# Performance work log

Hardware: AMD Instinct MI355X
Metric: run time of the kernel (lower is better)

## Reference

```python
import jax, jax.numpy as jnp
import numpy as np

B, S, D = 4, 4096, 1024

def setup_inputs() -> dict:
    key = jax.random.key(0)
    ks = jax.random.split(key, 7)
    scale = 1.0 / np.sqrt(D)
    X  = jax.random.normal(ks[0], (B, S, D), dtype=jnp.float32)
    Wq = jax.random.normal(ks[1], (D, D), dtype=jnp.float32) * scale
    bq = jnp.zeros((D,), dtype=jnp.float32)
    Wk = jax.random.normal(ks[2], (D, D), dtype=jnp.float32) * scale
    bk = jnp.zeros((D,), dtype=jnp.float32)
    Wv = jax.random.normal(ks[3], (D, D), dtype=jnp.float32) * scale
    bv = jnp.zeros((D,), dtype=jnp.float32)
    return {"X": X, "Wq": Wq, "bq": bq, "Wk": Wk, "bk": bk, "Wv": Wv, "bv": bv}

def reference(X, Wq, bq, Wk, bk, Wv, bv):
    # Linear projections (torch Linear: x @ W.T + b; here W stored as [D_in, D_out])
    Q = jnp.einsum('bsd,de->bse', X, Wq) + bq
    K = jnp.einsum('bsd,de->bse', X, Wk) + bk
    V = jnp.einsum('bsd,de->bse', X, Wv) + bv
    inv_sqrt_d = 1.0 / jnp.sqrt(jnp.float32(X.shape[-1]))
    scores = jnp.einsum('bqd,bkd->bqk', Q, K) * inv_sqrt_d  # [B,S,S]
    weights = jax.nn.sigmoid(scores)  # elementwise, no row normalization
    return jnp.einsum('bqk,bkd->bqd', weights, V)
```

## Files before the change

### kernel.cpp

```cpp
#include <hip/hip_runtime.h>
#include <hip/hip_bf16.h>

typedef __bf16 bf16_t;
typedef bf16_t bf16x8 __attribute__((ext_vector_type(8)));
typedef float f32x4 __attribute__((ext_vector_type(4)));

constexpr int D_DIM = 1024;
constexpr int S_DIM = 4096;
constexpr int B_DIM = 4;

__global__ void cast_f32_bf16(const float* __restrict__ in, bf16_t* __restrict__ out) {
  size_t i = ((size_t)blockIdx.x * blockDim.x + threadIdx.x) * 8;
  float4 a = *(const float4*)(in + i);
  float4 b = *(const float4*)(in + i + 4);
  bf16x8 o;
  o[0] = (bf16_t)a.x; o[1] = (bf16_t)a.y; o[2] = (bf16_t)a.z; o[3] = (bf16_t)a.w;
  o[4] = (bf16_t)b.x; o[5] = (bf16_t)b.y; o[6] = (bf16_t)b.z; o[7] = (bf16_t)b.w;
  *(bf16x8*)(out + i) = o;
}

__global__ void transpose_cast_1024(const float* __restrict__ in, bf16_t* __restrict__ out) {
  __shared__ float t[32][33];
  int x0 = blockIdx.x * 32, y0 = blockIdx.y * 32;
#pragma unroll
  for (int i = 0; i < 32; i += 8)
    t[threadIdx.y + i][threadIdx.x] =
        in[(size_t)(y0 + threadIdx.y + i) * D_DIM + (x0 + threadIdx.x)];
  __syncthreads();
#pragma unroll
  for (int i = 0; i < 32; i += 8)
    out[(size_t)(x0 + threadIdx.y + i) * D_DIM + (y0 + threadIdx.x)] =
        (bf16_t)t[threadIdx.x][threadIdx.y + i];
}

constexpr int BM2 = 256, BN2 = 256;

#define VMCNT8 asm volatile("s_waitcnt vmcnt(8)" ::: "memory")
#define VMCNT4 asm volatile("s_waitcnt vmcnt(4)" ::: "memory")
#define VMCNT0 asm volatile("s_waitcnt vmcnt(0)" ::: "memory")
#define LGKM8  asm volatile("s_waitcnt lgkmcnt(8)" ::: "memory")
#define LGKM0  asm volatile("s_waitcnt lgkmcnt(0)" ::: "memory")
#define SCHEDB __builtin_amdgcn_sched_barrier(0)
#define CFENCE asm volatile("" ::: "memory")
#define BAR __builtin_amdgcn_s_barrier()
#define PRIO1 __builtin_amdgcn_s_setprio(1)
#define PRIO0 __builtin_amdgcn_s_setprio(0)

__device__ __forceinline__ void stage_tile32(const bf16_t* __restrict__ g, int ld,
                                             bf16_t* lds, int tid) {
  const int w = tid >> 6, l = tid & 63;
  const int row = w * 16 + (l >> 2);
  const int chunk = (l & 3) * 8;
  const bf16_t* s0 = g + (size_t)row * ld + chunk;
  bf16_t* l0 = lds + w * 512;
  __builtin_amdgcn_global_load_lds((const __attribute__((address_space(1))) void*)s0,
                                   (__attribute__((address_space(3))) void*)l0, 16, 0, 0);
  __builtin_amdgcn_global_load_lds(
      (const __attribute__((address_space(1))) void*)(s0 + (size_t)128 * ld),
      (__attribute__((address_space(3))) void*)(l0 + 4096), 16, 0, 0);
}

template <int EPI, bool SWAP>
__global__ __launch_bounds__(512, 2) void gemm256k32(
    const bf16_t* __restrict__ A, const bf16_t* __restrict__ Bt,
    void* __restrict__ C0, void* __restrict__ C1, void* __restrict__ C2,
    const float* __restrict__ b0, const float* __restrict__ b1, const float* __restrict__ b2,
    int K, int lda, int ldb, int ldc, float scale,
    size_t sA, size_t sB, size_t sC) {
  __shared__ __align__(16) bf16_t smem[65536];

  const int tid = threadIdx.x;
  const int lane = tid & 63;
  const int w = tid >> 6;
  const int wr = (w >> 2) * 128;
  const int wc = (w & 3) * 64;
  const int fm = lane & 15;
  const int fko = (lane >> 4) * 8;

  const int nx = gridDim.x, ny = gridDim.y;
  const int nwg = nx * ny * gridDim.z;
  const int flat = blockIdx.x + nx * (blockIdx.y + ny * blockIdx.z);
  const int q = nwg >> 3;
  const int L = (flat & 7) * q + (flat >> 3);
  const int lx = L % nx;
  const int lt = L / nx;
  const int ly = lt % ny;
  const int lz = lt / ny;

  const int bx = SWAP ? ly : lx;
  const int by = SWAP ? lx : ly;

  const bf16_t* Ag = A + (size_t)lz * sA + (size_t)by * BM2 * lda;
  const bf16_t* Bg = Bt + (size_t)lz * sB + (size_t)bx * BN2 * ldb;

  f32x4 acc[8][4] = {};
  bf16x8 af[8], bfr[4];

  const int NT = K / 32;

  stage_tile32(Ag, lda, smem, tid);
  stage_tile32(Bg, ldb, smem + 8192, tid);
  stage_tile32(Ag + 32, lda, smem + 16384, tid);
  stage_tile32(Bg + 32, ldb, smem + 16384 + 8192, tid);
  stage_tile32(Ag + 64, lda, smem + 32768, tid);
  stage_tile32(Bg + 64, ldb, smem + 32768 + 8192, tid);
  VMCNT8;
  BAR;

#pragma unroll 1
  for (int t = 0; t < NT; ++t) {
    const bf16_t* As = smem + (t & 3) * 16384;
    const bf16_t* Bs = As + 8192;

#pragma unroll
    for (int m = 0; m < 8; ++m)
      af[m] = *(const bf16x8*)&As[(wr + m * 16 + fm) * 32 + fko];
#pragma unroll
    for (int n = 0; n < 4; ++n)
      bfr[n] = *(const bf16x8*)&Bs[(wc + n * 16 + fm) * 32 + fko];

    if (t + 3 < NT) {
      bf16_t* dst = smem + ((t + 3) & 3) * 16384;
      stage_tile32(Ag + (size_t)(t + 3) * 32, lda, dst, tid);
      stage_tile32(Bg + (size_t)(t + 3) * 32, ldb, dst + 8192, tid);
    }

    LGKM8; CFENCE; BAR;
    LGKM0; SCHEDB;
    PRIO1;
#pragma unroll
    for (int m = 0; m < 8; ++m)
#pragma unroll
      for (int n = 0; n < 4; ++n)
        acc[m][n] = __builtin_amdgcn_mfma_f32_16x16x32_bf16(af[m], bfr[n], acc[m][n], 0, 0, 0);
    PRIO0;

    const int rem = NT - 1 - t;
    if (rem >= 3) { VMCNT8; }
    else if (rem == 2) { VMCNT4; }
    else if (rem == 1) { VMCNT0; }
    BAR;
  }

  const int row0 = by * BM2 + wr + (lane >> 4) * 4;
  const int col0 = bx * BN2 + wc + fm;

  if constexpr (EPI == 0) {
    const int seg = bx >> 2;
    const float* bias = (seg == 0) ? b0 : (seg == 1) ? b1 : b2;
#pragma unroll
    for (int i = 0; i < 8; ++i) {
#pragma unroll
      for (int j = 0; j < 4; ++j) {
        const int n = col0 + j * 16;
        const int nl = n & 1023;
        const float bv = bias[nl];
#pragma unroll
        for (int r = 0; r < 4; ++r) {
          const int m = row0 + i * 16 + r;
          float v = acc[i][j][r] + bv;
          if (seg < 2) {
            bf16_t* C = (bf16_t*)(seg == 0 ? C0 : C1);
            C[(size_t)m * D_DIM + nl] = (bf16_t)v;
          } else {
            bf16_t* C = (bf16_t*)C2;
            C[((size_t)(m >> 12) << 22) + (size_t)nl * S_DIM + (m & (S_DIM - 1))] = (bf16_t)v;
          }
        }
      }
    }
  } else {
#pragma unroll
    for (int i = 0; i < 8; ++i) {
#pragma unroll
      for (int j = 0; j < 4; ++j) {
        const int n = col0 + j * 16;
#pragma unroll
        for (int r = 0; r < 4; ++r) {
          const int m = row0 + i * 16 + r;
          float v = acc[i][j][r];
          if constexpr (EPI == 2) {
            bf16_t* C = (bf16_t*)C0 + (size_t)lz * sC;
            float s = 1.0f / (1.0f + __expf(-v * scale));
            C[(size_t)m * ldc + n] = (bf16_t)s;
          } else {
            float* C = (float*)C0 + (size_t)lz * sC;
            C[(size_t)m * ldc + n] = v;
          }
        }
      }
    }
  }
}

extern "C" void kernel_launch(void* const* d_in, const int* in_sizes, int n_in,
                              void* d_out, int out_size, void* d_ws, size_t ws_size,
                              hipStream_t stream) {
  const float* X  = (const float*)d_in[0];
  const float* Wq = (const float*)d_in[1];
  const float* bq = (const float*)d_in[2];
  const float* Wk = (const float*)d_in[3];
  const float* bk = (const float*)d_in[4];
  const float* Wv = (const float*)d_in[5];
  const float* bv = (const float*)d_in[6];
  float* out = (float*)d_out;

  const int M = B_DIM * S_DIM;
  const size_t SD = (size_t)S_DIM * D_DIM;
  const size_t E  = (size_t)M * D_DIM;
  const size_t PE1 = (size_t)S_DIM * S_DIM;
  const size_t WE = (size_t)D_DIM * D_DIM;

  size_t need4 = (4 * PE1 + 3 * E + 3 * WE) * sizeof(bf16_t);
  const int PB = (ws_size >= need4) ? 4 : 1;
  const size_t psz = (size_t)PB * PE1;

  bf16_t* ws = (bf16_t*)d_ws;
  bf16_t* P   = ws;
  bf16_t* Xb  = ws;
  bf16_t* Qb  = ws + psz;
  bf16_t* Kb  = Qb + E;
  bf16_t* Vt  = Kb + E;
  bf16_t* Wt  = Vt + E;

  cast_f32_bf16<<<dim3((unsigned)(E / 8 / 256)), dim3(256), 0, stream>>>(X, Xb);

  dim3 tg(D_DIM / 32, D_DIM / 32), tb(32, 8);
  transpose_cast_1024<<<tg, tb, 0, stream>>>(Wq, Wt);
  transpose_cast_1024<<<tg, tb, 0, stream>>>(Wk, Wt + WE);
  transpose_cast_1024<<<tg, tb, 0, stream>>>(Wv, Wt + 2 * WE);

  dim3 pg(3 * D_DIM / BN2, M / BM2, 1);
  gemm256k32<0, false><<<pg, dim3(512), 0, stream>>>(
      Xb, Wt, Qb, Kb, Vt, bq, bk, bv, D_DIM, D_DIM, D_DIM, D_DIM, 1.0f, 0, 0, 0);

  const float scale = 0.03125f;
  for (int b0 = 0; b0 < B_DIM; b0 += PB) {
    dim3 sg(S_DIM / BN2, S_DIM / BM2, PB);
    gemm256k32<2, false><<<sg, dim3(512), 0, stream>>>(
        Qb + (size_t)b0 * SD, Kb + (size_t)b0 * SD, P,
        nullptr, nullptr, nullptr, nullptr, nullptr,
        D_DIM, D_DIM, D_DIM, S_DIM, scale, SD, SD, PE1);
    dim3 vg(S_DIM / BM2, D_DIM / BN2, PB);
    gemm256k32<3, true><<<vg, dim3(512), 0, stream>>>(
        P, Vt + (size_t)b0 * SD, out + (size_t)b0 * SD,
        nullptr, nullptr, nullptr, nullptr, nullptr,
        S_DIM, S_DIM, S_DIM, D_DIM, 1.0f, PE1, SD, SD);
  }
}
```

Before: 604.2 us.

## Switch GEMM to K=64 double-buffered tiles with XOR-swizzled LDS layout

The GEMM kernel now stages 64-wide K tiles into two LDS slots instead of 32-wide tiles in a four-deep ring, issuing two MFMA sub-steps per tile and prefetching two tiles ahead. The LDS layout is XOR-swizzled on row so that the 128-byte row stride no longer causes bank conflicts on fragment reads. This halves the number of loop iterations and barriers per K and aims to reduce LDS bank conflicts. In exchange, prefetch depth drops from three tiles to one, and LDS use doubles to 128 KB per block, which may limit occupancy to one block per CU despite launch_bounds(512,2).

```diff
diff --git a/kernel.cpp b/kernel.cpp
--- a/kernel.cpp
+++ b/kernel.cpp
@@ -34,40 +34,70 @@
 }
 
 constexpr int BM2 = 256, BN2 = 256;
+constexpr int SLOT = 65536;
 
 #define VMCNT8 asm volatile("s_waitcnt vmcnt(8)" ::: "memory")
-#define VMCNT4 asm volatile("s_waitcnt vmcnt(4)" ::: "memory")
 #define VMCNT0 asm volatile("s_waitcnt vmcnt(0)" ::: "memory")
-#define LGKM8  asm volatile("s_waitcnt lgkmcnt(8)" ::: "memory")
 #define LGKM0  asm volatile("s_waitcnt lgkmcnt(0)" ::: "memory")
 #define SCHEDB __builtin_amdgcn_sched_barrier(0)
-#define CFENCE asm volatile("" ::: "memory")
 #define BAR __builtin_amdgcn_s_barrier()
 #define PRIO1 __builtin_amdgcn_s_setprio(1)
 #define PRIO0 __builtin_amdgcn_s_setprio(0)
 
-__device__ __forceinline__ void stage_tile32(const bf16_t* __restrict__ g, int ld,
-                                             bf16_t* lds, int tid) {
+__device__ __forceinline__ void stage_half(const bf16_t* __restrict__ g, int ld,
+                                           char* lds, int tid) {
   const int w = tid >> 6, l = tid & 63;
-  const int row = w * 16 + (l >> 2);
-  const int chunk = (l & 3) * 8;
-  const bf16_t* s0 = g + (size_t)row * ld + chunk;
-  bf16_t* l0 = lds + w * 512;
+  const int rw = l >> 3;
+  const int gl = (l & 7) ^ rw;
+  char* l0 = lds + w * 1024;
+  const bf16_t* s0 = g + (size_t)(w * 8 + rw) * ld + gl * 8;
   __builtin_amdgcn_global_load_lds((const __attribute__((address_space(1))) void*)s0,
                                    (__attribute__((address_space(3))) void*)l0, 16, 0, 0);
   __builtin_amdgcn_global_load_lds(
-      (const __attribute__((address_space(1))) void*)(s0 + (size_t)128 * ld),
-      (__attribute__((address_space(3))) void*)(l0 + 4096), 16, 0, 0);
+      (const __attribute__((address_space(1))) void*)(s0 + (size_t)64 * ld),
+      (__attribute__((address_space(3))) void*)(l0 + 8192), 16, 0, 0);
+}
+
+__device__ __forceinline__ void stage_tile(const bf16_t* __restrict__ gA, int lda,
+                                           const bf16_t* __restrict__ gB, int ldb,
+                                           char* slot, int tid) {
+  stage_half(gA, lda, slot, tid);
+  stage_half(gA + (size_t)128 * lda, lda, slot + 16384, tid);
+  stage_half(gB, ldb, slot + 32768, tid);
+  stage_half(gB + (size_t)128 * ldb, ldb, slot + 49152, tid);
+}
+
+__device__ __forceinline__ void load_a8(const char* __restrict__ At, int wr, int fm,
+                                        int kx, bf16x8 (&af)[8]) {
+#pragma unroll
+  for (int m = 0; m < 8; ++m)
+    af[m] = *(const bf16x8*)(At + (wr + m * 16 + fm) * 128 + kx);
+}
+
+__device__ __forceinline__ void load_b4(const char* __restrict__ Bt_, int wc, int fm,
+                                        int kx, bf16x8 (&bfr)[4]) {
+#pragma unroll
+  for (int n = 0; n < 4; ++n)
+    bfr[n] = *(const bf16x8*)(Bt_ + (wc + n * 16 + fm) * 128 + kx);
+}
+
+__device__ __forceinline__ void mfma32(f32x4 (&acc)[8][4], const bf16x8 (&af)[8],
+                                       const bf16x8 (&bfr)[4]) {
+#pragma unroll
+  for (int m = 0; m < 8; ++m)
+#pragma unroll
+    for (int n = 0; n < 4; ++n)
+      acc[m][n] = __builtin_amdgcn_mfma_f32_16x16x32_bf16(af[m], bfr[n], acc[m][n], 0, 0, 0);
 }
 
 template <int EPI, bool SWAP>
-__global__ __launch_bounds__(512, 2) void gemm256k32(
+__global__ __launch_bounds__(512, 2) void gemm256f(
     const bf16_t* __restrict__ A, const bf16_t* __restrict__ Bt,
     void* __restrict__ C0, void* __restrict__ C1, void* __restrict__ C2,
     const float* __restrict__ b0, const float* __restrict__ b1, const float* __restrict__ b2,
     int K, int lda, int ldb, int ldc, float scale,
     size_t sA, size_t sB, size_t sC) {
-  __shared__ __align__(16) bf16_t smem[65536];
+  __shared__ __align__(16) char smem[2 * SLOT];
 
   const int tid = threadIdx.x;
   const int lane = tid & 63;
@@ -75,7 +105,10 @@
   const int wr = (w >> 2) * 128;
   const int wc = (w & 3) * 64;
   const int fm = lane & 15;
-  const int fko = (lane >> 4) * 8;
+  const int ssw = (fm & 7) << 4;
+  const int kp = (lane >> 4) << 4;
+  const int kxa = kp ^ ssw;
+  const int kxb = (64 | kp) ^ ssw;
 
   const int nx = gridDim.x, ny = gridDim.y;
   const int nwg = nx * ny * gridDim.z;
@@ -96,49 +129,33 @@
   f32x4 acc[8][4] = {};
   bf16x8 af[8], bfr[4];
 
-  const int NT = K / 32;
-
-  stage_tile32(Ag, lda, smem, tid);
-  stage_tile32(Bg, ldb, smem + 8192, tid);
-  stage_tile32(Ag + 32, lda, smem + 16384, tid);
-  stage_tile32(Bg + 32, ldb, smem + 16384 + 8192, tid);
-  stage_tile32(Ag + 64, lda, smem + 32768, tid);
-  stage_tile32(Bg + 64, ldb, smem + 32768 + 8192, tid);
+  const int NT = K / 64;
+
+  stage_tile(Ag, lda, Bg, ldb, smem, tid);
+  stage_tile(Ag + 64, lda, Bg + 64, ldb, smem + SLOT, tid);
   VMCNT8;
   BAR;
 
 #pragma unroll 1
   for (int t = 0; t < NT; ++t) {
-    const bf16_t* As = smem + (t & 3) * 16384;
-    const bf16_t* Bs = As + 8192;
-
-#pragma unroll
-    for (int m = 0; m < 8; ++m)
-      af[m] = *(const bf16x8*)&As[(wr + m * 16 + fm) * 32 + fko];
-#pragma unroll
-    for (int n = 0; n < 4; ++n)
-      bfr[n] = *(const bf16x8*)&Bs[(wc + n * 16 + fm) * 32 + fko];
-
-    if (t + 3 < NT) {
-      bf16_t* dst = smem + ((t + 3) & 3) * 16384;
-      stage_tile32(Ag + (size_t)(t + 3) * 32, lda, dst, tid);
-      stage_tile32(Bg + (size_t)(t + 3) * 32, ldb, dst + 8192, tid);
-    }
-
-    LGKM8; CFENCE; BAR;
+    const char* Aslot = smem + (t & 1) * SLOT;
+    const char* Bslot = Aslot + 32768;
+
+    load_a8(Aslot, wr, fm, kxa, af);
+    load_b4(Bslot, wc, fm, kxa, bfr);
     LGKM0; SCHEDB;
-    PRIO1;
-#pragma unroll
-    for (int m = 0; m < 8; ++m)
-#pragma unroll
-      for (int n = 0; n < 4; ++n)
-        acc[m][n] = __builtin_amdgcn_mfma_f32_16x16x32_bf16(af[m], bfr[n], acc[m][n], 0, 0, 0);
-    PRIO0;
-
-    const int rem = NT - 1 - t;
-    if (rem >= 3) { VMCNT8; }
-    else if (rem == 2) { VMCNT4; }
-    else if (rem == 1) { VMCNT0; }
+    PRIO1; mfma32(acc, af, bfr); PRIO0;
+
+    load_a8(Aslot, wr, fm, kxb, af);
+    load_b4(Bslot, wc, fm, kxb, bfr);
+    LGKM0; SCHEDB;
+    PRIO1; mfma32(acc, af, bfr); PRIO0;
+
+    BAR;
+    if (t + 2 < NT)
+      stage_tile(Ag + (size_t)(t + 2) * 64, lda, Bg + (size_t)(t + 2) * 64, ldb,
+                 (char*)smem + (t & 1) * SLOT, tid);
+    if (t + 1 < NT) { if (t + 2 < NT) { VMCNT8; } else { VMCNT0; } }
     BAR;
   }
 
@@ -231,18 +248,18 @@
   transpose_cast_1024<<<tg, tb, 0, stream>>>(Wv, Wt + 2 * WE);
 
   dim3 pg(3 * D_DIM / BN2, M / BM2, 1);
-  gemm256k32<0, false><<<pg, dim3(512), 0, stream>>>(
+  gemm256f<0, false><<<pg, dim3(512), 0, stream>>>(
       Xb, Wt, Qb, Kb, Vt, bq, bk, bv, D_DIM, D_DIM, D_DIM, D_DIM, 1.0f, 0, 0, 0);
 
   const float scale = 0.03125f;
   for (int b0 = 0; b0 < B_DIM; b0 += PB) {
     dim3 sg(S_DIM / BN2, S_DIM / BM2, PB);
-    gemm256k32<2, false><<<sg, dim3(512), 0, stream>>>(
+    gemm256f<2, false><<<sg, dim3(512), 0, stream>>>(
         Qb + (size_t)b0 * SD, Kb + (size_t)b0 * SD, P,
         nullptr, nullptr, nullptr, nullptr, nullptr,
         D_DIM, D_DIM, D_DIM, S_DIM, scale, SD, SD, PE1);
     dim3 vg(S_DIM / BM2, D_DIM / BN2, PB);
-    gemm256k32<3, true><<<vg, dim3(512), 0, stream>>>(
+    gemm256f<3, true><<<vg, dim3(512), 0, stream>>>(
         P, Vt + (size_t)b0 * SD, out + (size_t)b0 * SD,
         nullptr, nullptr, nullptr, nullptr, nullptr,
         S_DIM, S_DIM, S_DIM, D_DIM, 1.0f, PE1, SD, SD);
```

Measured after the change: 560.7 us. 7.2% less time.
